# Performance work log

Measured on AMD Instinct MI355X. Metric: run time of the kernel, lower is better.

Reference implementation:

```python
import jax, jax.numpy as jnp
import numpy as np

N, V, D, F, E, H = 10000, 4, 3, 128, 320000, 128
EDGE_IN = 2 * F + 2 * V  # node_features[senders] + node_features[receivers] + lengths_x^2 + lengths_y^2
NORM_CONST = 1.0


def setup_inputs() -> dict:
    key = jax.random.key(0)
    ks = jax.random.split(key, 20)
    w = lambda k, shape: jax.random.normal(k, shape, jnp.float32) * 0.05
    z = lambda n: jnp.zeros((n,), jnp.float32)
    return dict(
        node_positions=jax.random.normal(ks[0], (N, V, D), jnp.float32),
        node_vectors=jax.random.normal(ks[1], (N, V, D), jnp.float32),
        node_features=jax.random.normal(ks[2], (N, F), jnp.float32),
        senders=jax.random.randint(ks[3], (E,), 0, N),
        receivers=jax.random.randint(ks[4], (E,), 0, N),
        We0=w(ks[5], (EDGE_IN, H)), be0=z(H), We1=w(ks[6], (H, H)), be1=z(H),
        Winf=w(ks[7], (H, 1)), binf=z(1),
        Wx0=w(ks[8], (H, H)), bx0=z(H), Wx1=w(ks[9], (H, H)), bx1=z(H), Wxf=w(ks[10], (H, V)),
        Wy0=w(ks[11], (H, H)), by0=z(H), Wy1=w(ks[12], (H, H)), by1=z(H), Wyf=w(ks[13], (H, V)),
        Wh0=w(ks[14], (H + F, H)), bh0=z(H), Wh1=w(ks[15], (H, H)), bh1=z(H), Wh2=w(ks[16], (H, F)), bh2=z(F),
    )


def reference(node_positions, node_vectors, node_features, senders, receivers,
              We0, be0, We1, be1, Winf, binf,
              Wx0, bx0, Wx1, bx1, Wxf,
              Wy0, by0, Wy1, by1, Wyf,
              Wh0, bh0, Wh1, bh1, Wh2, bh2):
    act = jax.nn.silu
    n_nodes = node_positions.shape[0]
    avg = int(np.sqrt(receivers.shape[0]))  # avg_num_neighbours as in source

    def radial(coord):  # coord: [N, V, D]
        d = coord[receivers] - coord[senders]              # [E, V, D]
        l = jnp.sqrt(jnp.sum(d * d, axis=-1) + 1e-8)       # [E, V] safe_norm
        d = d / (NORM_CONST + l[:, :, None])               # normalize=True
        return l, d

    lx, dx = radial(node_positions)
    ly, dy = radial(node_vectors)

    ef = jnp.concatenate([node_features[senders], node_features[receivers],
                          lx ** 2, ly ** 2], axis=-1)      # [E, 264]
    m = act(act(ef @ We0 + be0) @ We1 + be1)               # phi_e, activate_final=True

    # phi_x: torso MLP + no-bias head, tanh
    px = jnp.tanh(act(act(m @ Wx0 + bx0) @ Wx1 + bx1) @ Wxf)          # [E, V]
    shifts_x = jax.ops.segment_sum(dx * px[:, :, None], receivers, num_segments=n_nodes) / avg

    # phi_y: torso MLP + no-bias head, tanh
    py = jnp.tanh(act(act(m @ Wy0 + by0) @ Wy1 + by1) @ Wyf)          # [E, V]
    shifts_y = jax.ops.segment_sum(dy * py[:, :, None], receivers, num_segments=n_nodes) / avg

    # attention gate on messages
    m = m * jax.nn.sigmoid(m @ Winf + binf)
    m_i = jax.ops.segment_sum(m, receivers, num_segments=n_nodes) / avg

    # phi_h (activate_final=False) + residual_h
    hin = jnp.concatenate([m_i, node_features], axis=-1)
    features_out = act(act(hin @ Wh0 + bh0) @ Wh1 + bh1) @ Wh2 + bh2 + node_features

    skip = shifts_y
    vectors_out = skip + node_vectors            # residual_y
    positions_out = shifts_x + node_positions    # x_update='x', residual_x
    return positions_out, vectors_out, features_out, skip
```

## Files before the change

### kernel.cpp

```cpp
#include <hip/hip_runtime.h>
#include <math.h>

#define NN 10000
#define EE 320000
#define TE 32
#define TN 16
#define INV_AVG (1.0f / 565.0f)

#define OUT_POS 0
#define OUT_VEC 120000
#define OUT_FEAT 240000
#define OUT_SKIP 1520000
#define OUT_TOTAL 1640000

#define WS_WE0 0
#define WS_WE1 36864
#define WS_WX0 53248
#define WS_WX1 69632
#define WS_WY0 86016
#define WS_WY1 102400
#define WS_WH0 118784
#define WS_WH1 151552
#define WS_WH2 167936
#define WS_WXF 184320
#define WS_WYF 186368
#define WS_OFF_NF 376832
#define WS_OFF_SORT 2936832
#define WS_OFF_CNT  4216832
#define WS_OFF_CUR  4256832

typedef __attribute__((ext_vector_type(8))) short bfrag;
typedef __attribute__((ext_vector_type(4))) float f4acc;

__device__ __forceinline__ float siluf(float x) {
    return x * __builtin_amdgcn_rcpf(1.0f + __expf(-x));
}
__device__ __forceinline__ float tanh_fast(float x) {
    return 1.0f - 2.0f * __builtin_amdgcn_rcpf(__expf(2.0f * x) + 1.0f);
}
__device__ __forceinline__ float sigmoid_fast(float x) {
    return __builtin_amdgcn_rcpf(1.0f + __expf(-x));
}
__device__ __forceinline__ unsigned int cvt_pk_bf16(float lo, float hi) {
    unsigned int r;
    asm("v_cvt_pk_bf16_f32 %0, %1, %2" : "=v"(r) : "v"(lo), "v"(hi));
    return r;
}
__device__ __forceinline__ unsigned short f2bf(float x) {
    union { float f; unsigned int u; } c; c.f = x;
    unsigned int r = c.u + 0x7FFFu + ((c.u >> 16) & 1u);
    return (unsigned short)(r >> 16);
}
__device__ __forceinline__ float bf2f(unsigned short h) {
    union { unsigned int u; float f; } c; c.u = ((unsigned int)h) << 16; return c.f;
}

__global__ __launch_bounds__(256) void init_kernel(const float* __restrict__ pos,
                                                   float* __restrict__ out,
                                                   int* __restrict__ cnt)
{
    int idx = blockIdx.x * 256 + threadIdx.x;
    if (idx < OUT_TOTAL) out[idx] = (idx < 120000) ? pos[idx] : 0.0f;
    if (idx < NN) cnt[idx] = 0;
}

__global__ __launch_bounds__(256) void prep_all(
    const float* __restrict__ nf, unsigned short* __restrict__ nfb,
    const int* __restrict__ rcv, int* __restrict__ cnt,
    const float* __restrict__ We0, const float* __restrict__ be0,
    const float* __restrict__ We1,
    const float* __restrict__ Wx0, const float* __restrict__ Wx1,
    const float* __restrict__ Wy0, const float* __restrict__ Wy1,
    const float* __restrict__ Wh0, const float* __restrict__ Wh1,
    const float* __restrict__ Wh2,
    const float* __restrict__ Wxf, const float* __restrict__ Wyf,
    unsigned short* __restrict__ wsW)
{
    int tid = blockIdx.x * 256 + threadIdx.x;
    int i = tid * 8;
    if (i < NN * 128) {
        float4 a = *(const float4*)(nf + i);
        float4 b = *(const float4*)(nf + i + 4);
        uint4 pk;
        pk.x = cvt_pk_bf16(a.x, a.y);
        pk.y = cvt_pk_bf16(a.z, a.w);
        pk.z = cvt_pk_bf16(b.x, b.y);
        pk.w = cvt_pk_bf16(b.z, b.w);
        *(uint4*)(nfb + i) = pk;
    }
    int e = tid * 2;
    if (e < EE) {
        atomicAdd(cnt + rcv[e], 1);
        atomicAdd(cnt + rcv[e + 1], 1);
    }
    if (tid >= 23552) return;
    if (tid >= 23040) {
        const float* Wf = (tid < 23296) ? Wxf : Wyf;
        unsigned short* dst = wsW + ((tid < 23296) ? WS_WXF : WS_WYF);
        int rel = tid - ((tid < 23296) ? 23040 : 23296);
        int kc = rel >> 6, lane = rel & 63;
        int lhi = lane >> 4, llo = lane & 15;
        unsigned short* o = dst + ((kc * 64 + lane) << 3);
#pragma unroll
        for (int j = 0; j < 8; ++j) {
            int k = kc * 32 + lhi * 8 + j;
            o[j] = (llo < 4) ? f2bf(Wf[k * 4 + llo]) : (unsigned short)0;
        }
        return;
    }
    const float* W; unsigned short* dst; int Kact = 128, rel; int isWe0 = 0;
    if (tid < 4608)        { W = We0; dst = wsW + WS_WE0; Kact = 264; rel = tid; isWe0 = 1; }
    else if (tid < 14848)  {
        int r = tid - 4608; int m = r >> 11; rel = r & 2047;
        switch (m) {
            case 0: W = We1; dst = wsW + WS_WE1; break;
            case 1: W = Wx0; dst = wsW + WS_WX0; break;
            case 2: W = Wx1; dst = wsW + WS_WX1; break;
            case 3: W = Wy0; dst = wsW + WS_WY0; break;
            default: W = Wy1; dst = wsW + WS_WY1; break;
        }
    }
    else if (tid < 18944)  { W = Wh0; dst = wsW + WS_WH0; Kact = 256; rel = tid - 14848; }
    else if (tid < 20992)  { W = Wh1; dst = wsW + WS_WH1; rel = tid - 18944; }
    else                   { W = Wh2; dst = wsW + WS_WH2; rel = tid - 20992; }
    int lane = rel & 63, oc = (rel >> 6) & 7, kc = rel >> 9;
    int k0 = kc * 32 + ((lane >> 4) << 3);
    int col = oc * 16 + (lane & 15);
    unsigned short* o = dst + (((kc * 8 + oc) * 64 + lane) << 3);
#pragma unroll
    for (int j = 0; j < 8; ++j) {
        int k = k0 + j;
        unsigned short v = 0;
        if (k < Kact) v = f2bf(W[k * 128 + col]);
        else if (isWe0 && k == 264) v = f2bf(be0[col]);
        o[j] = v;
    }
}

__global__ __launch_bounds__(1024) void scan_kernel(const int* __restrict__ cnt,
                                                    int* __restrict__ cursor)
{
    __shared__ int wsum[16];
    int t = threadIdx.x;
    int lane = t & 63, wid = t >> 6;
    int base = t * 10;
    int c[10];
    int s = 0;
#pragma unroll
    for (int i = 0; i < 10; ++i) {
        int b = base + i;
        c[i] = (b < NN) ? cnt[b] : 0;
        s += c[i];
    }
    int run = s;
#pragma unroll
    for (int off = 1; off < 64; off <<= 1) {
        int v = __shfl_up(run, off);
        if (lane >= off) run += v;
    }
    if (lane == 63) wsum[wid] = run;
    __syncthreads();
    if (t < 16) {
        int v = wsum[t];
#pragma unroll
        for (int off = 1; off < 16; off <<= 1) {
            int u = __shfl_up(v, off);
            if (t >= off) v += u;
        }
        wsum[t] = v;
    }
    __syncthreads();
    int wave_excl = (wid == 0) ? 0 : wsum[wid - 1];
    int excl = wave_excl + run - s;
#pragma unroll
    for (int i = 0; i < 10; ++i) {
        int b = base + i;
        if (b < NN) { cursor[b] = excl; excl += c[i]; }
    }
}

__global__ __launch_bounds__(256) void scatter_sort_kernel(const int* __restrict__ rcv,
                                                           int* __restrict__ cursor,
                                                           int* __restrict__ sortedIdx)
{
    int e = blockIdx.x * 256 + threadIdx.x;
    if (e < EE) {
        int slot = atomicAdd(cursor + rcv[e], 1);
        sortedIdx[slot] = e;
    }
}

template<int KC, int MT, int NT>
__device__ __forceinline__ void gemm_lds(const unsigned short* __restrict__ fragW,
                                         const unsigned short* Bld, const int bstride,
                                         const int tile0, const int lane,
                                         f4acc acc[MT][NT])
{
    const int lhi = lane >> 4, llo = lane & 15;
#pragma unroll
    for (int kc = 0; kc < KC; ++kc) {
        bfrag b[NT];
#pragma unroll
        for (int nt = 0; nt < NT; ++nt)
            b[nt] = *(const bfrag*)(Bld + (nt * 16 + llo) * bstride + kc * 32 + lhi * 8);
#pragma unroll
        for (int i = 0; i < MT; ++i) {
            bfrag a = *(const bfrag*)(fragW + (((kc * 8 + tile0 + i) * 64 + lane) << 3));
#pragma unroll
            for (int nt = 0; nt < NT; ++nt)
                acc[i][nt] = __builtin_amdgcn_mfma_f32_16x16x32_bf16(a, b[nt], acc[i][nt], 0, 0, 0);
        }
    }
}

template<int NT>
__device__ __forceinline__ void epilogue_silu_t(f4acc acc[2][NT], const float* __restrict__ bias,
                                                unsigned short* Dld, int lane, int w)
{
    const int lhi = lane >> 4, llo = lane & 15;
#pragma unroll
    for (int i = 0; i < 2; ++i) {
        int ch = (w * 2 + i) * 16 + lhi * 4;
        float4 bv = *(const float4*)(bias + ch);
#pragma unroll
        for (int nt = 0; nt < NT; ++nt) {
            uint2 pk;
            pk.x = cvt_pk_bf16(siluf(acc[i][nt][0] + bv.x), siluf(acc[i][nt][1] + bv.y));
            pk.y = cvt_pk_bf16(siluf(acc[i][nt][2] + bv.z), siluf(acc[i][nt][3] + bv.w));
            *(uint2*)(Dld + (nt * 16 + llo) * 136 + ch) = pk;
        }
    }
}

__device__ __forceinline__ void epilogue_silu_nobias(f4acc acc[2][2],
                                                     unsigned short* Dld, int lane, int w)
{
    const int lhi = lane >> 4, llo = lane & 15;
#pragma unroll
    for (int i = 0; i < 2; ++i) {
        int ch = (w * 2 + i) * 16 + lhi * 4;
#pragma unroll
        for (int nt = 0; nt < 2; ++nt) {
            uint2 pk;
            pk.x = cvt_pk_bf16(siluf(acc[i][nt][0]), siluf(acc[i][nt][1]));
            pk.y = cvt_pk_bf16(siluf(acc[i][nt][2]), siluf(acc[i][nt][3]));
            *(uint2*)(Dld + (nt * 16 + llo) * 136 + ch) = pk;
        }
    }
}

__global__ __launch_bounds__(256, 4) void edge_kernel(
    const float* __restrict__ pos, const float* __restrict__ vec,
    const unsigned short* __restrict__ nfb,
    const int* __restrict__ snd, const int* __restrict__ rcv,
    const int* __restrict__ sortedIdx,
    const unsigned short* __restrict__ wsW,
    const float* __restrict__ be1,
    const float* __restrict__ Winf, const float* __restrict__ binf,
    const float* __restrict__ bx0, const float* __restrict__ bx1,
    const float* __restrict__ by0, const float* __restrict__ by1,
    float* outPos, float* outSkip, float* outFeat)
{
    __shared__ unsigned short L2T[TE * 40];
    __shared__ unsigned short H0[TE * 136];
    __shared__ unsigned short Hm[TE * 136];
    __shared__ unsigned short H2[TE * 136];
    __shared__ float dstore[TE * 24];
    __shared__ float pxy[TE * 8];
    __shared__ float gateacc[TE];
    __shared__ int sidx[TE], ridx[TE];

    const int t = threadIdx.x;
    const int lane = t & 63, w = t >> 6;
    const int lhi = lane >> 4, llo = lane & 15;
    const int e_base = blockIdx.x * TE;

    if (t < TE) {
        int eid = sortedIdx[e_base + t];
        int sn = snd[eid], rn = rcv[eid];
        sidx[t] = sn; ridx[t] = rn;
#pragma unroll
        for (int tensor = 0; tensor < 2; ++tensor) {
            const float* c = tensor ? vec : pos;
#pragma unroll
            for (int v = 0; v < 4; ++v) {
                float d0 = c[rn * 12 + v * 3 + 0] - c[sn * 12 + v * 3 + 0];
                float d1 = c[rn * 12 + v * 3 + 1] - c[sn * 12 + v * 3 + 1];
                float d2 = c[rn * 12 + v * 3 + 2] - c[sn * 12 + v * 3 + 2];
                float ss = fmaf(d0, d0, fmaf(d1, d1, d2 * d2)) + 1e-8f;
                float l = sqrtf(ss);
                float inv = __builtin_amdgcn_rcpf(1.0f + l);
                L2T[t * 40 + tensor * 4 + v] = f2bf(ss);
                dstore[t * 24 + tensor * 12 + v * 3 + 0] = d0 * inv;
                dstore[t * 24 + tensor * 12 + v * 3 + 1] = d1 * inv;
                dstore[t * 24 + tensor * 12 + v * 3 + 2] = d2 * inv;
            }
        }
#pragma unroll
        for (int j = 0; j < 6; ++j)
            *(uint2*)(L2T + t * 40 + 8 + j * 4) = make_uint2(0u, 0u);
        L2T[t * 40 + 8] = 0x3F80u;
    }
    if (t >= 64 && t < 96) gateacc[t - 64] = 0.0f;
    __syncthreads();

    {
        const int sn0 = sidx[llo], sn1 = sidx[16 + llo];
        const int rn0 = ridx[llo], rn1 = ridx[16 + llo];
        const unsigned short* s0 = nfb + sn0 * 128 + lhi * 8;
        const unsigned short* s1 = nfb + sn1 * 128 + lhi * 8;
        const unsigned short* r0 = nfb + rn0 * 128 + lhi * 8;
        const unsigned short* r1 = nfb + rn1 * 128 + lhi * 8;
        const int mt0 = w * 2;
        f4acc acc[2][2];
#pragma unroll
        for (int i = 0; i < 2; ++i) { acc[i][0] = (f4acc){0.f,0.f,0.f,0.f}; acc[i][1] = (f4acc){0.f,0.f,0.f,0.f}; }
#pragma unroll
        for (int kc = 0; kc < 8; ++kc) {
            bfrag b0 = *(const bfrag*)((kc < 4 ? s0 : r0) + (kc & 3) * 32);
            bfrag b1 = *(const bfrag*)((kc < 4 ? s1 : r1) + (kc & 3) * 32);
#pragma unroll
            for (int i = 0; i < 2; ++i) {
                bfrag a = *(const bfrag*)(wsW + WS_WE0 + (((kc * 8 + mt0 + i) * 64 + lane) << 3));
                acc[i][0] = __builtin_amdgcn_mfma_f32_16x16x32_bf16(a, b0, acc[i][0], 0, 0, 0);
                acc[i][1] = __builtin_amdgcn_mfma_f32_16x16x32_bf16(a, b1, acc[i][1], 0, 0, 0);
            }
        }
        {
            bfrag b0 = *(const bfrag*)(L2T + llo * 40 + lhi * 8);
            bfrag b1 = *(const bfrag*)(L2T + (16 + llo) * 40 + lhi * 8);
#pragma unroll
            for (int i = 0; i < 2; ++i) {
                bfrag a = *(const bfrag*)(wsW + WS_WE0 + (((8 * 8 + mt0 + i) * 64 + lane) << 3));
                acc[i][0] = __builtin_amdgcn_mfma_f32_16x16x32_bf16(a, b0, acc[i][0], 0, 0, 0);
                acc[i][1] = __builtin_amdgcn_mfma_f32_16x16x32_bf16(a, b1, acc[i][1], 0, 0, 0);
            }
        }
        epilogue_silu_nobias(acc, H0, lane, w);
    }
    __syncthreads();

    {
        f4acc acc[2][2];
#pragma unroll
        for (int i = 0; i < 2; ++i) { acc[i][0] = (f4acc){0.f,0.f,0.f,0.f}; acc[i][1] = (f4acc){0.f,0.f,0.f,0.f}; }
        gemm_lds<4, 2, 2>(wsW + WS_WE1, H0, 136, w * 2, lane, acc);
        float gp0 = 0.0f, gp1 = 0.0f;
#pragma unroll
        for (int i = 0; i < 2; ++i) {
            int ch = (w * 2 + i) * 16 + lhi * 4;
            float4 bv = *(const float4*)(be1 + ch);
            float4 wg = *(const float4*)(Winf + ch);
#pragma unroll
            for (int nt = 0; nt < 2; ++nt) {
                float v0 = siluf(acc[i][nt][0] + bv.x);
                float v1 = siluf(acc[i][nt][1] + bv.y);
                float v2 = siluf(acc[i][nt][2] + bv.z);
                float v3 = siluf(acc[i][nt][3] + bv.w);
                uint2 pk;
                pk.x = cvt_pk_bf16(v0, v1);
                pk.y = cvt_pk_bf16(v2, v3);
                *(uint2*)(Hm + (nt * 16 + llo) * 136 + ch) = pk;
                float g = fmaf(v0, wg.x, fmaf(v1, wg.y, fmaf(v2, wg.z, v3 * wg.w)));
                if (nt == 0) gp0 += g; else gp1 += g;
            }
        }
        gp0 += __shfl_xor(gp0, 16); gp0 += __shfl_xor(gp0, 32);
        gp1 += __shfl_xor(gp1, 16); gp1 += __shfl_xor(gp1, 32);
        if (lane < 16) {
            atomicAdd(&gateacc[lane], gp0);
            atomicAdd(&gateacc[16 + lane], gp1);
        }
    }
    __syncthreads();

    {
        f4acc acc[2][2];
#pragma unroll
        for (int i = 0; i < 2; ++i) { acc[i][0] = (f4acc){0.f,0.f,0.f,0.f}; acc[i][1] = (f4acc){0.f,0.f,0.f,0.f}; }
        gemm_lds<4, 2, 2>(wsW + WS_WX0, Hm, 136, w * 2, lane, acc);
        epilogue_silu_t<2>(acc, bx0, H0, lane, w);
    }
    __syncthreads();

    {
        f4acc acc[2][2];
#pragma unroll
        for (int i = 0; i < 2; ++i) { acc[i][0] = (f4acc){0.f,0.f,0.f,0.f}; acc[i][1] = (f4acc){0.f,0.f,0.f,0.f}; }
        gemm_lds<4, 2, 2>(wsW + WS_WX1, H0, 136, w * 2, lane, acc);
        epilogue_silu_t<2>(acc, bx1, H2, lane, w);
    }
    __syncthreads();

    {
        f4acc acc[2][2];
#pragma unroll
        for (int i = 0; i < 2; ++i) { acc[i][0] = (f4acc){0.f,0.f,0.f,0.f}; acc[i][1] = (f4acc){0.f,0.f,0.f,0.f}; }
        gemm_lds<4, 2, 2>(wsW + WS_WY0, Hm, 136, w * 2, lane, acc);
        epilogue_silu_t<2>(acc, by0, H0, lane, w);
        if (w < 2) {
            f4acc h = (f4acc){0.f, 0.f, 0.f, 0.f};
#pragma unroll
            for (int kc = 0; kc < 4; ++kc) {
                bfrag b = *(const bfrag*)(H2 + (w * 16 + llo) * 136 + kc * 32 + lhi * 8);
                bfrag a = *(const bfrag*)(wsW + WS_WXF + ((kc * 64 + lane) << 3));
                h = __builtin_amdgcn_mfma_f32_16x16x32_bf16(a, b, h, 0, 0, 0);
            }
            if (lhi == 0) {
#pragma unroll
                for (int v = 0; v < 4; ++v)
                    pxy[(w * 16 + llo) * 8 + v] = h[v];
            }
        }
    }
    __syncthreads();

    {
        f4acc acc[2][2];
#pragma unroll
        for (int i = 0; i < 2; ++i) { acc[i][0] = (f4acc){0.f,0.f,0.f,0.f}; acc[i][1] = (f4acc){0.f,0.f,0.f,0.f}; }
        gemm_lds<4, 2, 2>(wsW + WS_WY1, H0, 136, w * 2, lane, acc);
        epilogue_silu_t<2>(acc, by1, H2, lane, w);
    }
    __syncthreads();

    if (w < 2) {
        f4acc h = (f4acc){0.f, 0.f, 0.f, 0.f};
#pragma unroll
        for (int kc = 0; kc < 4; ++kc) {
            bfrag b = *(const bfrag*)(H2 + (w * 16 + llo) * 136 + kc * 32 + lhi * 8);
            bfrag a = *(const bfrag*)(wsW + WS_WYF + ((kc * 64 + lane) << 3));
            h = __builtin_amdgcn_mfma_f32_16x16x32_bf16(a, b, h, 0, 0, 0);
        }
        if (lhi == 0) {
#pragma unroll
            for (int v = 0; v < 4; ++v)
                pxy[(w * 16 + llo) * 8 + 4 + v] = h[v];
        }
    }
    __syncthreads();

    pxy[t] = tanh_fast(pxy[t]) * INV_AVG;
    if (t < TE) gateacc[t] = sigmoid_fast(gateacc[t] + binf[0]) * INV_AVG;
    __syncthreads();

    if (t < 128) {
        int half = t >> 6, pair = t & 63;
        int jj = pair * 2;
        int e0h = half * 16;
        float a0 = 0.0f, a1 = 0.0f;
        int prev_r = ridx[e0h];
#pragma unroll
        for (int i = 0; i < 16; ++i) {
            int e = e0h + i;
            int r = ridx[e];
            if (r != prev_r) {
                atomicAdd(outFeat + prev_r * 128 + jj, a0);
                atomicAdd(outFeat + prev_r * 128 + jj + 1, a1);
                a0 = a1 = 0.0f;
                prev_r = r;
            }
            unsigned int pk = *(const unsigned int*)(Hm + e * 136 + jj);
            float g = gateacc[e];
            a0 = fmaf(bf2f((unsigned short)(pk & 0xffffu)), g, a0);
            a1 = fmaf(bf2f((unsigned short)(pk >> 16)), g, a1);
        }
        atomicAdd(outFeat + prev_r * 128 + jj, a0);
        atomicAdd(outFeat + prev_r * 128 + jj + 1, a1);
    } else if (t >= 208) {
        int s = t - 208;
        int c = s >> 1, half = s & 1;
        int tensor = (c >= 12) ? 1 : 0;
        int rem = c - tensor * 12;
        int v = rem / 3;
        float* dstp = tensor ? outSkip : outPos;
        int e0h = half * 16;
        float acc = 0.0f;
        int prev_r = ridx[e0h];
#pragma unroll
        for (int i = 0; i < 16; ++i) {
            int e = e0h + i;
            int r = ridx[e];
            if (r != prev_r) {
                atomicAdd(dstp + prev_r * 12 + rem, acc);
                acc = 0.0f;
                prev_r = r;
            }
            acc = fmaf(dstore[e * 24 + c], pxy[e * 8 + tensor * 4 + v], acc);
        }
        atomicAdd(dstp + prev_r * 12 + rem, acc);
    }
}

__global__ __launch_bounds__(256) void node_kernel(
    const float* __restrict__ nf, const unsigned short* __restrict__ nfb,
    const float* __restrict__ nvec,
    const unsigned short* __restrict__ wsW,
    const float* __restrict__ bh0, const float* __restrict__ bh1,
    const float* __restrict__ bh2,
    float* outFeat , float* outVec,
    const float* __restrict__ outSkip)
{
    __shared__ unsigned short A[TN * 264];
    __shared__ unsigned short H1[TN * 136];
    __shared__ unsigned short H2b[TN * 136];
    const int t = threadIdx.x;
    const int lane = t & 63, w = t >> 6;
    const int lhi = lane >> 4, llo = lane & 15;
    const int n_base = blockIdx.x * TN;

#pragma unroll
    for (int it = 0; it < 4; ++it) {
        int idx = t + it * 256;
        int row = idx >> 6, q = idx & 63;
        int n = n_base + row;
        float2 v = make_float2(0.f, 0.f);
        if (n < NN) v = *(const float2*)(outFeat + n * 128 + q * 2);
        *(unsigned int*)(A + row * 264 + q * 2) = cvt_pk_bf16(v.x, v.y);
    }
    {
        int row = t >> 4, q = t & 15;
        int n = n_base + row;
        uint4 v = make_uint4(0u, 0u, 0u, 0u);
        if (n < NN) v = *(const uint4*)(nfb + n * 128 + q * 8);
        *(uint4*)(A + row * 264 + 128 + q * 8) = v;
    }
    __syncthreads();
    {
        f4acc acc[2][1];
        acc[0][0] = (f4acc){0.f,0.f,0.f,0.f}; acc[1][0] = (f4acc){0.f,0.f,0.f,0.f};
        gemm_lds<8, 2, 1>(wsW + WS_WH0, A, 264, w * 2, lane, acc);
        epilogue_silu_t<1>(acc, bh0, H1, lane, w);
    }
    __syncthreads();
    {
        f4acc acc[2][1];
        acc[0][0] = (f4acc){0.f,0.f,0.f,0.f}; acc[1][0] = (f4acc){0.f,0.f,0.f,0.f};
        gemm_lds<4, 2, 1>(wsW + WS_WH1, H1, 136, w * 2, lane, acc);
        epilogue_silu_t<1>(acc, bh1, H2b, lane, w);
    }
    __syncthreads();
    {
        f4acc acc[2][1];
        acc[0][0] = (f4acc){0.f,0.f,0.f,0.f}; acc[1][0] = (f4acc){0.f,0.f,0.f,0.f};
        gemm_lds<4, 2, 1>(wsW + WS_WH2, H2b, 136, w * 2, lane, acc);
#pragma unroll
        for (int i = 0; i < 2; ++i) {
            int ch = (w * 2 + i) * 16 + lhi * 4;
            float4 bv = *(const float4*)(bh2 + ch);
            int n = n_base + llo;
            if (n < NN) {
                float4 r = *(const float4*)(nf + n * 128 + ch);
                float4 o;
                o.x = acc[i][0][0] + bv.x + r.x;
                o.y = acc[i][0][1] + bv.y + r.y;
                o.z = acc[i][0][2] + bv.z + r.z;
                o.w = acc[i][0][3] + bv.w + r.w;
                *(float4*)(outFeat + n * 128 + ch) = o;
            }
        }
    }
    if (t < TN * 12) {
        int n = n_base + t / 12;
        if (n < NN) {
            int g = n_base * 12 + t;
            outVec[g] = outSkip[g] + nvec[g];
        }
    }
}

extern "C" void kernel_launch(void* const* d_in, const int* in_sizes, int n_in,
                              void* d_out, int out_size, void* d_ws, size_t ws_size,
                              hipStream_t stream)
{
    (void)in_sizes; (void)n_in; (void)out_size; (void)ws_size;

    const float* pos  = (const float*)d_in[0];
    const float* vecv = (const float*)d_in[1];
    const float* nf   = (const float*)d_in[2];
    const int*   snd  = (const int*)d_in[3];
    const int*   rcv  = (const int*)d_in[4];
    const float* We0  = (const float*)d_in[5];
    const float* be0  = (const float*)d_in[6];
    const float* We1  = (const float*)d_in[7];
    const float* be1  = (const float*)d_in[8];
    const float* Winf = (const float*)d_in[9];
    const float* binf = (const float*)d_in[10];
    const float* Wx0  = (const float*)d_in[11];
    const float* bx0  = (const float*)d_in[12];
    const float* Wx1  = (const float*)d_in[13];
    const float* bx1  = (const float*)d_in[14];
    const float* Wxf  = (const float*)d_in[15];
    const float* Wy0  = (const float*)d_in[16];
    const float* by0  = (const float*)d_in[17];
    const float* Wy1  = (const float*)d_in[18];
    const float* by1  = (const float*)d_in[19];
    const float* Wyf  = (const float*)d_in[20];
    const float* Wh0  = (const float*)d_in[21];
    const float* bh0  = (const float*)d_in[22];
    const float* Wh1  = (const float*)d_in[23];
    const float* bh1  = (const float*)d_in[24];
    const float* Wh2  = (const float*)d_in[25];
    const float* bh2  = (const float*)d_in[26];

    float* out     = (float*)d_out;
    float* outPos  = out + OUT_POS;
    float* outVec  = out + OUT_VEC;
    float* outFeat = out + OUT_FEAT;
    float* outSkip = out + OUT_SKIP;

    char* ws = (char*)d_ws;
    unsigned short* wsW = (unsigned short*)ws;
    unsigned short* nfb = (unsigned short*)(ws + WS_OFF_NF);
    int* sortedIdx      = (int*)(ws + WS_OFF_SORT);
    int* cnt            = (int*)(ws + WS_OFF_CNT);
    int* cursor         = (int*)(ws + WS_OFF_CUR);

    init_kernel<<<(OUT_TOTAL + 255) / 256, 256, 0, stream>>>(pos, out, cnt);

    prep_all<<<(NN * 128 / 8 + 255) / 256, 256, 0, stream>>>(
        nf, nfb, rcv, cnt,
        We0, be0, We1, Wx0, Wx1, Wy0, Wy1, Wh0, Wh1, Wh2, Wxf, Wyf, wsW);

    scan_kernel<<<1, 1024, 0, stream>>>(cnt, cursor);
    scatter_sort_kernel<<<(EE + 255) / 256, 256, 0, stream>>>(rcv, cursor, sortedIdx);

    edge_kernel<<<EE / TE, 256, 0, stream>>>(
        pos, vecv, nfb, snd, rcv, sortedIdx, wsW,
        be1, Winf, binf,
        bx0, bx1, by0, by1,
        outPos, outSkip, outFeat);

    node_kernel<<<(NN + TN - 1) / TN, 256, 0, stream>>>(
        nf, nfb, vecv, wsW, bh0, bh1, bh2,
        outFeat, outVec, outSkip);
}
```

Baseline: 258.7 us.

## Drop H2 LDS buffer, loop x/y branches, raise launch-bounds occupancy

Removes the third shared-memory activation buffer by running the x and y MLP branches in a non-unrolled loop and writing the second layer's output back into H0 in place, with an extra barrier between the GEMM reads and the epilogue writes. Less LDS per block and a launch-bounds hint raised from 4 to 6 blocks per SM are meant to let more blocks stay resident and hide gather latency. In exchange, the x and y branches no longer interleave (the old code ran the y first layer alongside the x head), an extra __syncthreads is added per branch, and the register cap may cause spills.

```diff
diff --git a/kernel.cpp b/kernel.cpp
--- a/kernel.cpp
+++ b/kernel.cpp
@@ -249,7 +249,7 @@
     }
 }
 
-__global__ __launch_bounds__(256, 4) void edge_kernel(
+__global__ __launch_bounds__(256, 6) void edge_kernel(
     const float* __restrict__ pos, const float* __restrict__ vec,
     const unsigned short* __restrict__ nfb,
     const int* __restrict__ snd, const int* __restrict__ rcv,
@@ -264,7 +264,6 @@
     __shared__ unsigned short L2T[TE * 40];
     __shared__ unsigned short H0[TE * 136];
     __shared__ unsigned short Hm[TE * 136];
-    __shared__ unsigned short H2[TE * 136];
     __shared__ float dstore[TE * 24];
     __shared__ float pxy[TE * 8];
     __shared__ float gateacc[TE];
@@ -374,71 +373,46 @@
     }
     __syncthreads();
 
-    {
-        f4acc acc[2][2];
-#pragma unroll
-        for (int i = 0; i < 2; ++i) { acc[i][0] = (f4acc){0.f,0.f,0.f,0.f}; acc[i][1] = (f4acc){0.f,0.f,0.f,0.f}; }
-        gemm_lds<4, 2, 2>(wsW + WS_WX0, Hm, 136, w * 2, lane, acc);
-        epilogue_silu_t<2>(acc, bx0, H0, lane, w);
-    }
-    __syncthreads();
-
-    {
-        f4acc acc[2][2];
-#pragma unroll
-        for (int i = 0; i < 2; ++i) { acc[i][0] = (f4acc){0.f,0.f,0.f,0.f}; acc[i][1] = (f4acc){0.f,0.f,0.f,0.f}; }
-        gemm_lds<4, 2, 2>(wsW + WS_WX1, H0, 136, w * 2, lane, acc);
-        epilogue_silu_t<2>(acc, bx1, H2, lane, w);
-    }
-    __syncthreads();
-
-    {
-        f4acc acc[2][2];
-#pragma unroll
-        for (int i = 0; i < 2; ++i) { acc[i][0] = (f4acc){0.f,0.f,0.f,0.f}; acc[i][1] = (f4acc){0.f,0.f,0.f,0.f}; }
-        gemm_lds<4, 2, 2>(wsW + WS_WY0, Hm, 136, w * 2, lane, acc);
-        epilogue_silu_t<2>(acc, by0, H0, lane, w);
+#pragma unroll 1
+    for (int br = 0; br < 2; ++br) {
+        {
+            const unsigned short* fw = wsW + (br ? WS_WY0 : WS_WX0);
+            const float* bias = br ? by0 : bx0;
+            f4acc acc[2][2];
+#pragma unroll
+            for (int i = 0; i < 2; ++i) { acc[i][0] = (f4acc){0.f,0.f,0.f,0.f}; acc[i][1] = (f4acc){0.f,0.f,0.f,0.f}; }
+            gemm_lds<4, 2, 2>(fw, Hm, 136, w * 2, lane, acc);
+            epilogue_silu_t<2>(acc, bias, H0, lane, w);
+        }
+        __syncthreads();
+        {
+            const unsigned short* fw = wsW + (br ? WS_WY1 : WS_WX1);
+            const float* bias = br ? by1 : bx1;
+            f4acc acc[2][2];
+#pragma unroll
+            for (int i = 0; i < 2; ++i) { acc[i][0] = (f4acc){0.f,0.f,0.f,0.f}; acc[i][1] = (f4acc){0.f,0.f,0.f,0.f}; }
+            gemm_lds<4, 2, 2>(fw, H0, 136, w * 2, lane, acc);
+            __syncthreads();
+            epilogue_silu_t<2>(acc, bias, H0, lane, w);
+        }
+        __syncthreads();
         if (w < 2) {
+            const unsigned short* fw = wsW + (br ? WS_WYF : WS_WXF);
             f4acc h = (f4acc){0.f, 0.f, 0.f, 0.f};
 #pragma unroll
             for (int kc = 0; kc < 4; ++kc) {
-                bfrag b = *(const bfrag*)(H2 + (w * 16 + llo) * 136 + kc * 32 + lhi * 8);
-                bfrag a = *(const bfrag*)(wsW + WS_WXF + ((kc * 64 + lane) << 3));
+                bfrag b = *(const bfrag*)(H0 + (w * 16 + llo) * 136 + kc * 32 + lhi * 8);
+                bfrag a = *(const bfrag*)(fw + ((kc * 64 + lane) << 3));
                 h = __builtin_amdgcn_mfma_f32_16x16x32_bf16(a, b, h, 0, 0, 0);
             }
             if (lhi == 0) {
 #pragma unroll
                 for (int v = 0; v < 4; ++v)
-                    pxy[(w * 16 + llo) * 8 + v] = h[v];
-            }
-        }
-    }
-    __syncthreads();
-
-    {
-        f4acc acc[2][2];
-#pragma unroll
-        for (int i = 0; i < 2; ++i) { acc[i][0] = (f4acc){0.f,0.f,0.f,0.f}; acc[i][1] = (f4acc){0.f,0.f,0.f,0.f}; }
-        gemm_lds<4, 2, 2>(wsW + WS_WY1, H0, 136, w * 2, lane, acc);
-        epilogue_silu_t<2>(acc, by1, H2, lane, w);
-    }
-    __syncthreads();
-
-    if (w < 2) {
-        f4acc h = (f4acc){0.f, 0.f, 0.f, 0.f};
-#pragma unroll
-        for (int kc = 0; kc < 4; ++kc) {
-            bfrag b = *(const bfrag*)(H2 + (w * 16 + llo) * 136 + kc * 32 + lhi * 8);
-            bfrag a = *(const bfrag*)(wsW + WS_WYF + ((kc * 64 + lane) << 3));
-            h = __builtin_amdgcn_mfma_f32_16x16x32_bf16(a, b, h, 0, 0, 0);
-        }
-        if (lhi == 0) {
-#pragma unroll
-            for (int v = 0; v < 4; ++v)
-                pxy[(w * 16 + llo) * 8 + 4 + v] = h[v];
-        }
-    }
-    __syncthreads();
+                    pxy[(w * 16 + llo) * 8 + br * 4 + v] = h[v];
+            }
+        }
+        __syncthreads();
+    }
 
     pxy[t] = tanh_fast(pxy[t]) * INV_AVG;
     if (t < TE) gateacc[t] = sigmoid_fast(gateacc[t] + binf[0]) * INV_AVG;
```

After: 234.3 us (median of 2 runs). 1.1x faster.
